# Performance work log

Hardware: AMD Instinct MI355X
Metric: run time of the kernel (lower is better)

## Reference

```python
import jax, jax.numpy as jnp
import numpy as np

WARMUP = 5

def _smooth_l1(x):
    a = jnp.abs(x)
    return jnp.where(a < 1.0, 0.5 * a * a, a - 0.5)


def setup_inputs() -> dict:
    key = jax.random.key(0)
    ks = jax.random.split(key, 6)
    B, S, N, M, C = 8, 4, 8192, 50, 10
    return dict(
        pred_boxes=jax.random.normal(ks[0], (B, S, N, 7), jnp.float32),
        pred_classes=jax.random.normal(ks[1], (B, S, N, C), jnp.float32),
        pred_scores=jax.random.normal(ks[2], (B, S, N), jnp.float32),
        gt_boxes=jax.random.normal(ks[3], (B, M, 7), jnp.float32) * 3.0,
        gt_classes=jax.random.randint(ks[4], (B, M), 0, C),
        n_gt=jax.random.randint(ks[5], (B,), 1, M + 1),
        w_center=jnp.float32(2.0),   # loss_weights['center']
        w_obj=jnp.float32(0.5),      # loss_weights['obj']
        w_unmatched=jnp.float32(5.0),# loss_weights['unmatched']
        epoch=0,
    )


def _forward(pred_boxes, pred_classes, pred_scores, gt_boxes, gt_classes, n_gt, w_center, w_obj, w_unmatched, epoch):
    # epoch < WARMUP path: k_factor=10, use_objectness=False, distance_threshold=5.0, cls_weight=0
    K_FACTOR = 10
    COST_THRESH = 5.0 * 10.0  # distance_threshold * 10
    B, S, N, _ = pred_boxes.shape
    M = gt_boxes.shape[1]
    gt_mask = jnp.arange(M)[None, :] < n_gt[:, None]            # [B,M] valid (non-padded) GTs

    pc = pred_boxes[..., :3]                                    # [B,S,N,3]
    gc = gt_boxes[..., :3]                                      # [B,M,3]
    diff = pc[:, :, :, None, :] - gc[:, None, None, :, :]       # [B,S,N,M,3]
    dist = jnp.sqrt(jnp.sum(diff * diff, axis=-1))              # [B,S,N,M] center L2 cost

    # ---- progressive matching (vectorized over B,S,GT) ----
    cost = jnp.where(gt_mask[:, None, None, :], dist, jnp.inf)
    masked = jnp.where(cost < COST_THRESH, cost, jnp.inf)
    neg = -jnp.swapaxes(masked, -1, -2)                         # [B,S,M,N]
    vals, idx = jax.lax.top_k(neg, K_FACTOR)                    # k smallest costs per gt
    pick_ok = vals > -jnp.inf                                   # [B,S,M,k] valid picks
    gt_ids = jnp.broadcast_to(jnp.arange(M, dtype=jnp.int32)[None, None, :, None], idx.shape)
    bidx = jnp.broadcast_to(jnp.arange(B)[:, None, None, None], idx.shape)
    sidx = jnp.broadcast_to(jnp.arange(S)[None, :, None, None], idx.shape)
    assign = jnp.full((B, S, N), -1, dtype=jnp.int32)
    assign = assign.at[bidx, sidx, idx].max(jnp.where(pick_ok, gt_ids, -1))
    matched_gt = pick_ok.any(-1)                                # [B,S,M]
    unmatched = gt_mask[:, None, :] & ~matched_gt               # [B,S,M]

    # ---- center loss (smooth-L1 over matched query/GT center pairs) ----
    pos = assign >= 0                                           # [B,S,N]
    a = jnp.maximum(assign, 0)
    gtc = gc[jnp.arange(B)[:, None, None], a]                   # [B,S,N,3]
    n_pos = pos.sum().astype(jnp.float32)
    loss_center = jnp.sum(_smooth_l1(pc - gtc) * pos[..., None]) / jnp.maximum(n_pos * 3.0, 1.0)

    # ---- progressive objectness loss (BCE-with-logits + dynamic pos_weight) ----
    t = pos.astype(pred_scores.dtype)
    n_neg = jnp.float32(t.size) - n_pos
    pw = jnp.minimum(10.0, n_neg / jnp.maximum(n_pos, 1.0))     # epoch < warmup branch
    x = pred_scores
    loss_obj = jnp.mean(pw * t * jax.nn.softplus(-x) + (1.0 - t) * jax.nn.softplus(x))

    # ---- unmatched-GT loss: pull 5 nearest predictions toward each unmatched GT ----
    dist_t = jnp.swapaxes(dist, -1, -2)                         # [B,S,M,N]
    nd, ni = jax.lax.top_k(-dist_t, 5)
    nd = -nd                                                    # 5 smallest distances [B,S,M,5]
    b5 = jnp.broadcast_to(jnp.arange(B)[:, None, None, None], ni.shape)
    s5 = jnp.broadcast_to(jnp.arange(S)[None, :, None, None], ni.shape)
    obj5 = pred_scores[b5, s5, ni]                              # [B,S,M,5]
    per_gt = jnp.mean(jnp.exp(-nd / 2.0) * (1.0 - obj5), axis=-1)
    per_gt = jnp.where(unmatched, per_gt, 0.0)
    n_entries = jnp.sum(unmatched.any(-1)).astype(jnp.float32)  # number of (b,s) pairs with unmatched gts
    loss_unm = per_gt.sum() / jnp.maximum(n_entries, 1.0)

    return loss_center * w_center + loss_obj * w_obj + loss_unm * w_unmatched


def reference(pred_boxes, pred_classes, pred_scores, gt_boxes, gt_classes, n_gt, w_center, w_obj, w_unmatched, epoch):
    return _forward(pred_boxes, pred_classes, pred_scores, gt_boxes, gt_classes, n_gt, w_center, w_obj, w_unmatched, epoch)
```

## Files before the change

### kernel.cpp

```cpp
#include <hip/hip_runtime.h>

#define NB 8
#define NS 4
#define NN 8192
#define NM 50
#define K10 10
#define THREADS 256
#define COST_THRESH 50.0f
#define LOSS_BLOCKS 256
#define NBUCK 1024
#define CAP 1024

__device__ __forceinline__ bool lexless(float d1, int i1, float d2, int i2) {
  return (d1 < d2) || (d1 == d2 && i1 < i2);
}

__global__ void __launch_bounds__(256) init_kernel(int* __restrict__ assign,
                                                   float* __restrict__ acc,
                                                   int* __restrict__ bs_unm) {
  int i = blockIdx.x * blockDim.x + threadIdx.x;
  const int total = NB * NS * NN;
  for (int j = i; j < total; j += gridDim.x * blockDim.x) assign[j] = -1;
  if (i == 0) acc[0] = 0.0f;
  if (i >= 64 && i < 64 + NB * NS) bs_unm[i - 64] = 0;
}

__global__ void __launch_bounds__(256) topk_kernel(
    const float* __restrict__ pred_boxes, const float* __restrict__ pred_scores,
    const float* __restrict__ gt_boxes, const int* __restrict__ n_gt,
    int* __restrict__ assign, float* __restrict__ per_gt_sum,
    int* __restrict__ bs_unm) {
  const int blk = blockIdx.x;
  const int m = blk % NM;
  const int bs = blk / NM;
  const int b = bs / NS;
  const int t = threadIdx.x;

  __shared__ float sd2[NN];
  __shared__ int shist[NBUCK];
  __shared__ float scd[CAP];
  __shared__ int sci[CAP];
  __shared__ float sred[16];
  __shared__ float sbb[2];
  __shared__ int scnt;
  __shared__ int sbucket;
  __shared__ float soutd[K10];
  __shared__ int souti[K10];

  for (int i = t; i < NBUCK; i += THREADS) shist[i] = 0;
  if (t == 0) { scnt = 0; sbucket = NBUCK - 2; }

  const float gx = gt_boxes[(b * NM + m) * 7 + 0];
  const float gy = gt_boxes[(b * NM + m) * 7 + 1];
  const float gz = gt_boxes[(b * NM + m) * 7 + 2];
  const bool valid = (m < n_gt[b]);

  const float* pb = pred_boxes + (size_t)bs * NN * 7;
  float lmin = INFINITY, lmax = 0.0f;
#pragma unroll
  for (int k = 0; k < NN / THREADS; k++) {
    int n = t + k * THREADS;
    float dx = pb[n * 7 + 0] - gx;
    float dy = pb[n * 7 + 1] - gy;
    float dz = pb[n * 7 + 2] - gz;
    float d2 = dx * dx + dy * dy + dz * dz;
    sd2[n] = d2;
    lmin = fminf(lmin, d2);
    lmax = fmaxf(lmax, d2);
  }
#pragma unroll
  for (int off = 32; off >= 1; off >>= 1) {
    lmin = fminf(lmin, __shfl_down(lmin, off));
    lmax = fmaxf(lmax, __shfl_down(lmax, off));
  }
  int wave = t >> 6;
  if ((t & 63) == 0) { sred[wave] = lmin; sred[8 + wave] = lmax; }
  __syncthreads();
  if (t == 0) {
    float bmin = fminf(fminf(sred[0], sred[1]), fminf(sred[2], sred[3]));
    float bmax = fmaxf(fmaxf(sred[8], sred[9]), fmaxf(sred[10], sred[11]));
    sbb[0] = bmin;
    sbb[1] = (float)NBUCK / fmaxf(bmax - bmin, 1e-30f);
  }
  __syncthreads();
  const float bmin = sbb[0], scale = sbb[1];

#pragma unroll
  for (int k = 0; k < NN / THREADS; k++) {
    int n = t + k * THREADS;
    int bidx = (int)((sd2[n] - bmin) * scale);
    bidx = min(NBUCK - 1, max(0, bidx));
    atomicAdd(&shist[bidx], 1);
  }
  __syncthreads();

  if (t < 64) {
    int lsum = 0;
    for (int i = 0; i < NBUCK / 64; i++) lsum += shist[t * (NBUCK / 64) + i];
    int incl = lsum;
#pragma unroll
    for (int off = 1; off < 64; off <<= 1) {
      int v = __shfl_up(incl, off);
      if (t >= off) incl += v;
    }
    int excl = incl - lsum;
    if (excl < K10 && incl >= K10) {
      int c = excl;
      for (int i = 0; i < NBUCK / 64; i++) {
        c += shist[t * (NBUCK / 64) + i];
        if (c >= K10) { sbucket = t * (NBUCK / 64) + i; break; }
      }
    }
  }
  __syncthreads();
  const float bound = bmin + ((float)(sbucket + 2) + 0.5f) / scale;

#pragma unroll
  for (int k = 0; k < NN / THREADS; k++) {
    int n = t + k * THREADS;
    float d2 = sd2[n];
    if (d2 < bound) {
      int p = atomicAdd(&scnt, 1);
      if (p < CAP) { scd[p] = d2; sci[p] = n; }
    }
  }
  __syncthreads();
  const int K = min(scnt, CAP);

  for (int c = t; c < K; c += THREADS) scd[c] = sqrtf(scd[c]);
  __syncthreads();
  for (int c = t; c < K; c += THREADS) {
    float dc = scd[c];
    int ic = sci[c];
    int rank = 0;
    for (int o = 0; o < K; o++) rank += lexless(scd[o], sci[o], dc, ic) ? 1 : 0;
    if (rank < K10) { soutd[rank] = dc; souti[rank] = ic; }
  }
  __syncthreads();

  if (t == 0) {
    bool matched = false;
#pragma unroll
    for (int k = 0; k < K10; k++) {
      if (valid && soutd[k] < COST_THRESH) {
        matched = true;
        atomicMax(&assign[(size_t)bs * NN + souti[k]], m);
      }
    }
    if (valid && !matched) {
      const float* ps = pred_scores + (size_t)bs * NN;
      float a = 0.0f;
#pragma unroll
      for (int k = 0; k < 5; k++) a += expf(-0.5f * soutd[k]) * (1.0f - ps[souti[k]]);
      atomicAdd(per_gt_sum, a * 0.2f);
      atomicOr(&bs_unm[bs], 1);
    }
  }
}

__global__ void __launch_bounds__(256) loss_kernel(
    const float* __restrict__ pred_boxes, const float* __restrict__ pred_scores,
    const float* __restrict__ gt_boxes, const int* __restrict__ assign,
    float* __restrict__ partials) {
  int tid = blockIdx.x * blockDim.x + threadIdx.x;
  const int total = NB * NS * NN;
  float lc = 0.0f, spp = 0.0f, spn = 0.0f, np = 0.0f;
  for (int i = tid; i < total; i += gridDim.x * blockDim.x) {
    int a = assign[i];
    float x = pred_scores[i];
    if (a >= 0) {
      np += 1.0f;
      int b = i / (NS * NN);
      const float* pbp = &pred_boxes[(size_t)i * 7];
      const float* gbp = &gt_boxes[(b * NM + a) * 7];
#pragma unroll
      for (int c = 0; c < 3; c++) {
        float diff = pbp[c] - gbp[c];
        float ad = fabsf(diff);
        lc += (ad < 1.0f) ? 0.5f * ad * ad : (ad - 0.5f);
      }
      spp += log1pf(expf(-fabsf(x))) + fmaxf(-x, 0.0f);
    } else {
      spn += log1pf(expf(-fabsf(x))) + fmaxf(x, 0.0f);
    }
  }
#pragma unroll
  for (int off = 32; off >= 1; off >>= 1) {
    lc += __shfl_down(lc, off);
    spp += __shfl_down(spp, off);
    spn += __shfl_down(spn, off);
    np += __shfl_down(np, off);
  }
  __shared__ float red[4][4];
  int wave = threadIdx.x >> 6;
  if ((threadIdx.x & 63) == 0) {
    red[wave][0] = lc; red[wave][1] = spp; red[wave][2] = spn; red[wave][3] = np;
  }
  __syncthreads();
  if (threadIdx.x == 0) {
    float o0 = 0, o1 = 0, o2 = 0, o3 = 0;
#pragma unroll
    for (int w = 0; w < 4; w++) { o0 += red[w][0]; o1 += red[w][1]; o2 += red[w][2]; o3 += red[w][3]; }
    float* p = &partials[(size_t)blockIdx.x * 8];
    p[0] = o0; p[1] = o1; p[2] = o2; p[3] = o3;
  }
}

__global__ void __launch_bounds__(256) final_kernel(
    const float* __restrict__ partials, const float* __restrict__ acc,
    const int* __restrict__ bs_unm,
    const float* __restrict__ wc, const float* __restrict__ wo,
    const float* __restrict__ wu, float* __restrict__ out) {
  const int t = threadIdx.x;
  const float* p = &partials[(size_t)t * 8];
  float lc = p[0], spp = p[1], spn = p[2], np = p[3];
#pragma unroll
  for (int off = 32; off >= 1; off >>= 1) {
    lc += __shfl_down(lc, off);
    spp += __shfl_down(spp, off);
    spn += __shfl_down(spn, off);
    np += __shfl_down(np, off);
  }
  __shared__ float red[4][4];
  int wave = t >> 6;
  if ((t & 63) == 0) {
    red[wave][0] = lc; red[wave][1] = spp; red[wave][2] = spn; red[wave][3] = np;
  }
  __syncthreads();
  if (t == 0) {
    float o0 = 0, o1 = 0, o2 = 0, o3 = 0;
#pragma unroll
    for (int w = 0; w < 4; w++) { o0 += red[w][0]; o1 += red[w][1]; o2 += red[w][2]; o3 += red[w][3]; }
    int ne = 0;
    for (int i = 0; i < NB * NS; i++) ne += bs_unm[i];
    float n_pos = o3;
    float loss_center = o0 / fmaxf(n_pos * 3.0f, 1.0f);
    float n_neg = (float)(NB * NS * NN) - n_pos;
    float pw = fminf(10.0f, n_neg / fmaxf(n_pos, 1.0f));
    float loss_obj = (pw * o1 + o2) / (float)(NB * NS * NN);
    float loss_unm = acc[0] / fmaxf((float)ne, 1.0f);
    out[0] = loss_center * wc[0] + loss_obj * wo[0] + loss_unm * wu[0];
  }
}

extern "C" void kernel_launch(void* const* d_in, const int* in_sizes, int n_in,
                              void* d_out, int out_size, void* d_ws, size_t ws_size,
                              hipStream_t stream) {
  const float* pred_boxes = (const float*)d_in[0];
  const float* pred_scores = (const float*)d_in[2];
  const float* gt_boxes = (const float*)d_in[3];
  const int* n_gt = (const int*)d_in[5];
  const float* wc = (const float*)d_in[6];
  const float* wo = (const float*)d_in[7];
  const float* wu = (const float*)d_in[8];
  float* out = (float*)d_out;

  char* ws = (char*)d_ws;
  int* assign = (int*)ws;
  float* acc = (float*)(ws + (size_t)NB * NS * NN * 4);
  int* bs_unm = (int*)((char*)acc + 256);
  float* partials = (float*)((char*)bs_unm + 256);

  init_kernel<<<256, 256, 0, stream>>>(assign, acc, bs_unm);
  topk_kernel<<<NB * NS * NM, THREADS, 0, stream>>>(pred_boxes, pred_scores, gt_boxes,
                                                    n_gt, assign, &acc[0], bs_unm);
  loss_kernel<<<LOSS_BLOCKS, 256, 0, stream>>>(pred_boxes, pred_scores, gt_boxes, assign, partials);
  final_kernel<<<1, 256, 0, stream>>>(partials, acc, bs_unm, wc, wo, wu, out);
}
```

Measured before the change: 45.30 us.

## Pack box centers into SoA, fuse final reduction, parallelize match epilogue

A prep kernel now transposes the xyz centers of pred_boxes into a structure-of-arrays buffer, so the topk kernel (1600 blocks, each rereading its whole (b,s) slice) loads with coalesced unit stride instead of stride-7. The final reduction kernel is folded into the loss kernel through a last-block ticket counter, which removes one launch. The per-GT epilogue now uses one wavefront with __any and shuffles instead of a serial single thread. CAP drops from 1024 to 256, which shrinks shared memory and the O(K^2) rank loop but makes candidate overflow more likely.

```diff
diff --git a/kernel.cpp b/kernel.cpp
--- a/kernel.cpp
+++ b/kernel.cpp
@@ -9,24 +9,30 @@
 #define COST_THRESH 50.0f
 #define LOSS_BLOCKS 256
 #define NBUCK 1024
-#define CAP 1024
+#define CAP 256
+#define TOTAL (NB * NS * NN)
 
 __device__ __forceinline__ bool lexless(float d1, int i1, float d2, int i2) {
   return (d1 < d2) || (d1 == d2 && i1 < i2);
 }
 
-__global__ void __launch_bounds__(256) init_kernel(int* __restrict__ assign,
-                                                   float* __restrict__ acc,
-                                                   int* __restrict__ bs_unm) {
+__global__ void __launch_bounds__(256) prep_kernel(
+    const float* __restrict__ pred_boxes, float* __restrict__ packed,
+    int* __restrict__ assign, float* __restrict__ acc,
+    int* __restrict__ bs_unm, int* __restrict__ done) {
   int i = blockIdx.x * blockDim.x + threadIdx.x;
-  const int total = NB * NS * NN;
-  for (int j = i; j < total; j += gridDim.x * blockDim.x) assign[j] = -1;
-  if (i == 0) acc[0] = 0.0f;
+  for (int j = i; j < TOTAL; j += gridDim.x * blockDim.x) {
+    assign[j] = -1;
+    packed[j] = pred_boxes[j * 7 + 0];
+    packed[TOTAL + j] = pred_boxes[j * 7 + 1];
+    packed[2 * TOTAL + j] = pred_boxes[j * 7 + 2];
+  }
+  if (i == 0) { acc[0] = 0.0f; *done = 0; }
   if (i >= 64 && i < 64 + NB * NS) bs_unm[i - 64] = 0;
 }
 
 __global__ void __launch_bounds__(256) topk_kernel(
-    const float* __restrict__ pred_boxes, const float* __restrict__ pred_scores,
+    const float* __restrict__ packed, const float* __restrict__ pred_scores,
     const float* __restrict__ gt_boxes, const int* __restrict__ n_gt,
     int* __restrict__ assign, float* __restrict__ per_gt_sum,
     int* __restrict__ bs_unm) {
@@ -55,14 +61,17 @@
   const float gz = gt_boxes[(b * NM + m) * 7 + 2];
   const bool valid = (m < n_gt[b]);
 
-  const float* pb = pred_boxes + (size_t)bs * NN * 7;
+  const float* px = packed + (size_t)bs * NN;
+  const float* py = px + TOTAL;
+  const float* pz = py + TOTAL;
+
   float lmin = INFINITY, lmax = 0.0f;
 #pragma unroll
   for (int k = 0; k < NN / THREADS; k++) {
     int n = t + k * THREADS;
-    float dx = pb[n * 7 + 0] - gx;
-    float dy = pb[n * 7 + 1] - gy;
-    float dz = pb[n * 7 + 2] - gz;
+    float dx = px[n] - gx;
+    float dy = py[n] - gy;
+    float dz = pz[n] - gz;
     float d2 = dx * dx + dy * dy + dz * dz;
     sd2[n] = d2;
     lmin = fminf(lmin, d2);
@@ -138,44 +147,42 @@
   }
   __syncthreads();
 
-  if (t == 0) {
-    bool matched = false;
-#pragma unroll
-    for (int k = 0; k < K10; k++) {
-      if (valid && soutd[k] < COST_THRESH) {
-        matched = true;
-        atomicMax(&assign[(size_t)bs * NN + souti[k]], m);
+  if (t < 64) {
+    bool pick = (t < K10) && valid && (soutd[t] < COST_THRESH);
+    if (pick) atomicMax(&assign[(size_t)bs * NN + souti[t]], m);
+    bool matched = __any(pick);
+    if (valid && !matched) {
+      float a = 0.0f;
+      if (t < 5) a = expf(-0.5f * soutd[t]) * (1.0f - pred_scores[(size_t)bs * NN + souti[t]]);
+#pragma unroll
+      for (int off = 8; off >= 1; off >>= 1) a += __shfl_down(a, off);
+      if (t == 0) {
+        atomicAdd(per_gt_sum, a * 0.2f);
+        atomicOr(&bs_unm[bs], 1);
       }
     }
-    if (valid && !matched) {
-      const float* ps = pred_scores + (size_t)bs * NN;
-      float a = 0.0f;
-#pragma unroll
-      for (int k = 0; k < 5; k++) a += expf(-0.5f * soutd[k]) * (1.0f - ps[souti[k]]);
-      atomicAdd(per_gt_sum, a * 0.2f);
-      atomicOr(&bs_unm[bs], 1);
-    }
-  }
-}
-
-__global__ void __launch_bounds__(256) loss_kernel(
-    const float* __restrict__ pred_boxes, const float* __restrict__ pred_scores,
+  }
+}
+
+__global__ void __launch_bounds__(256) loss_final_kernel(
+    const float* __restrict__ packed, const float* __restrict__ pred_scores,
     const float* __restrict__ gt_boxes, const int* __restrict__ assign,
-    float* __restrict__ partials) {
+    float* __restrict__ partials, int* __restrict__ done,
+    const float* __restrict__ acc, const int* __restrict__ bs_unm,
+    const float* __restrict__ wc, const float* __restrict__ wo,
+    const float* __restrict__ wu, float* __restrict__ out) {
   int tid = blockIdx.x * blockDim.x + threadIdx.x;
-  const int total = NB * NS * NN;
   float lc = 0.0f, spp = 0.0f, spn = 0.0f, np = 0.0f;
-  for (int i = tid; i < total; i += gridDim.x * blockDim.x) {
+  for (int i = tid; i < TOTAL; i += gridDim.x * blockDim.x) {
     int a = assign[i];
     float x = pred_scores[i];
     if (a >= 0) {
       np += 1.0f;
       int b = i / (NS * NN);
-      const float* pbp = &pred_boxes[(size_t)i * 7];
       const float* gbp = &gt_boxes[(b * NM + a) * 7];
 #pragma unroll
       for (int c = 0; c < 3; c++) {
-        float diff = pbp[c] - gbp[c];
+        float diff = packed[c * TOTAL + i] - gbp[c];
         float ad = fabsf(diff);
         lc += (ad < 1.0f) ? 0.5f * ad * ad : (ad - 0.5f);
       }
@@ -192,6 +199,7 @@
     np += __shfl_down(np, off);
   }
   __shared__ float red[4][4];
+  __shared__ int s_last;
   int wave = threadIdx.x >> 6;
   if ((threadIdx.x & 63) == 0) {
     red[wave][0] = lc; red[wave][1] = spp; red[wave][2] = spn; red[wave][3] = np;
@@ -202,44 +210,48 @@
 #pragma unroll
     for (int w = 0; w < 4; w++) { o0 += red[w][0]; o1 += red[w][1]; o2 += red[w][2]; o3 += red[w][3]; }
     float* p = &partials[(size_t)blockIdx.x * 8];
-    p[0] = o0; p[1] = o1; p[2] = o2; p[3] = o3;
-  }
-}
-
-__global__ void __launch_bounds__(256) final_kernel(
-    const float* __restrict__ partials, const float* __restrict__ acc,
-    const int* __restrict__ bs_unm,
-    const float* __restrict__ wc, const float* __restrict__ wo,
-    const float* __restrict__ wu, float* __restrict__ out) {
-  const int t = threadIdx.x;
-  const float* p = &partials[(size_t)t * 8];
-  float lc = p[0], spp = p[1], spn = p[2], np = p[3];
-#pragma unroll
-  for (int off = 32; off >= 1; off >>= 1) {
-    lc += __shfl_down(lc, off);
-    spp += __shfl_down(spp, off);
-    spn += __shfl_down(spn, off);
-    np += __shfl_down(np, off);
-  }
-  __shared__ float red[4][4];
-  int wave = t >> 6;
-  if ((t & 63) == 0) {
-    red[wave][0] = lc; red[wave][1] = spp; red[wave][2] = spn; red[wave][3] = np;
-  }
-  __syncthreads();
-  if (t == 0) {
-    float o0 = 0, o1 = 0, o2 = 0, o3 = 0;
-#pragma unroll
-    for (int w = 0; w < 4; w++) { o0 += red[w][0]; o1 += red[w][1]; o2 += red[w][2]; o3 += red[w][3]; }
-    int ne = 0;
-    for (int i = 0; i < NB * NS; i++) ne += bs_unm[i];
-    float n_pos = o3;
-    float loss_center = o0 / fmaxf(n_pos * 3.0f, 1.0f);
-    float n_neg = (float)(NB * NS * NN) - n_pos;
-    float pw = fminf(10.0f, n_neg / fmaxf(n_pos, 1.0f));
-    float loss_obj = (pw * o1 + o2) / (float)(NB * NS * NN);
-    float loss_unm = acc[0] / fmaxf((float)ne, 1.0f);
-    out[0] = loss_center * wc[0] + loss_obj * wo[0] + loss_unm * wu[0];
+    __hip_atomic_store(&p[0], o0, __ATOMIC_RELAXED, __HIP_MEMORY_SCOPE_AGENT);
+    __hip_atomic_store(&p[1], o1, __ATOMIC_RELAXED, __HIP_MEMORY_SCOPE_AGENT);
+    __hip_atomic_store(&p[2], o2, __ATOMIC_RELAXED, __HIP_MEMORY_SCOPE_AGENT);
+    __hip_atomic_store(&p[3], o3, __ATOMIC_RELAXED, __HIP_MEMORY_SCOPE_AGENT);
+    __threadfence();
+    int ticket = __hip_atomic_fetch_add(done, 1, __ATOMIC_ACQ_REL, __HIP_MEMORY_SCOPE_AGENT);
+    s_last = (ticket == gridDim.x - 1) ? 1 : 0;
+  }
+  __syncthreads();
+  if (s_last) {
+    __threadfence();
+    const int t = threadIdx.x;
+    float l0 = __hip_atomic_load(&partials[t * 8 + 0], __ATOMIC_RELAXED, __HIP_MEMORY_SCOPE_AGENT);
+    float l1 = __hip_atomic_load(&partials[t * 8 + 1], __ATOMIC_RELAXED, __HIP_MEMORY_SCOPE_AGENT);
+    float l2 = __hip_atomic_load(&partials[t * 8 + 2], __ATOMIC_RELAXED, __HIP_MEMORY_SCOPE_AGENT);
+    float l3 = __hip_atomic_load(&partials[t * 8 + 3], __ATOMIC_RELAXED, __HIP_MEMORY_SCOPE_AGENT);
+#pragma unroll
+    for (int off = 32; off >= 1; off >>= 1) {
+      l0 += __shfl_down(l0, off);
+      l1 += __shfl_down(l1, off);
+      l2 += __shfl_down(l2, off);
+      l3 += __shfl_down(l3, off);
+    }
+    __shared__ float red2[4][4];
+    if ((t & 63) == 0) {
+      red2[t >> 6][0] = l0; red2[t >> 6][1] = l1; red2[t >> 6][2] = l2; red2[t >> 6][3] = l3;
+    }
+    __syncthreads();
+    if (t == 0) {
+      float o0 = 0, o1 = 0, o2 = 0, o3 = 0;
+#pragma unroll
+      for (int w = 0; w < 4; w++) { o0 += red2[w][0]; o1 += red2[w][1]; o2 += red2[w][2]; o3 += red2[w][3]; }
+      int ne = 0;
+      for (int i = 0; i < NB * NS; i++) ne += bs_unm[i];
+      float n_pos = o3;
+      float loss_center = o0 / fmaxf(n_pos * 3.0f, 1.0f);
+      float n_neg = (float)TOTAL - n_pos;
+      float pw = fminf(10.0f, n_neg / fmaxf(n_pos, 1.0f));
+      float loss_obj = (pw * o1 + o2) / (float)TOTAL;
+      float loss_unm = acc[0] / fmaxf((float)ne, 1.0f);
+      out[0] = loss_center * wc[0] + loss_obj * wo[0] + loss_unm * wu[0];
+    }
   }
 }
 
@@ -257,13 +269,15 @@
 
   char* ws = (char*)d_ws;
   int* assign = (int*)ws;
-  float* acc = (float*)(ws + (size_t)NB * NS * NN * 4);
-  int* bs_unm = (int*)((char*)acc + 256);
-  float* partials = (float*)((char*)bs_unm + 256);
-
-  init_kernel<<<256, 256, 0, stream>>>(assign, acc, bs_unm);
-  topk_kernel<<<NB * NS * NM, THREADS, 0, stream>>>(pred_boxes, pred_scores, gt_boxes,
+  float* packed = (float*)(ws + (size_t)TOTAL * 4);
+  float* acc = (float*)(ws + (size_t)TOTAL * 16);
+  int* done = (int*)((char*)acc + 64);
+  int* bs_unm = (int*)((char*)acc + 128);
+  float* partials = (float*)((char*)acc + 512);
+
+  prep_kernel<<<512, 256, 0, stream>>>(pred_boxes, packed, assign, acc, bs_unm, done);
+  topk_kernel<<<NB * NS * NM, THREADS, 0, stream>>>(packed, pred_scores, gt_boxes,
                                                     n_gt, assign, &acc[0], bs_unm);
-  loss_kernel<<<LOSS_BLOCKS, 256, 0, stream>>>(pred_boxes, pred_scores, gt_boxes, assign, partials);
-  final_kernel<<<1, 256, 0, stream>>>(partials, acc, bs_unm, wc, wo, wu, out);
-}
+  loss_final_kernel<<<LOSS_BLOCKS, 256, 0, stream>>>(packed, pred_scores, gt_boxes, assign,
+                                                     partials, done, acc, bs_unm, wc, wo, wu, out);
+}
```

Measured after the change: 48.15 us. +6.3%, slower.
